# Kernel optimization log

Hardware: AMD Instinct MI355X
Metric: run time of the kernel (lower is better)

## Reference

```python
import jax, jax.numpy as jnp
import numpy as np

N = 100_000   # nodes
E = 1_600_000 # edges (avg degree 16)
D = 32        # feat_dim


def setup_inputs() -> dict:
    key = jax.random.key(0)
    ks = jax.random.split(key, 8)
    scale = 1.0 / np.sqrt(D).astype(np.float32)
    feat = jax.random.normal(ks[0], (N, D), dtype=jnp.float32)
    src = jax.random.randint(ks[1], (E,), 0, N, dtype=jnp.int32)
    dst = jax.random.randint(ks[2], (E,), 0, N, dtype=jnp.int32)
    Ws = jax.random.normal(ks[3], (D, D), dtype=jnp.float32) * scale  # src_trans, no bias
    Wd = jax.random.normal(ks[4], (D, D), dtype=jnp.float32) * scale  # dst_trans
    bd = jax.random.normal(ks[5], (D,), dtype=jnp.float32) * scale
    Wr = jax.random.normal(ks[6], (D, D), dtype=jnp.float32) * scale  # res_trans
    br = jax.random.normal(ks[7], (D,), dtype=jnp.float32) * scale
    return {"feat": feat, "src": src, "dst": dst,
            "Ws": Ws, "Wd": Wd, "bd": bd, "Wr": Wr, "br": br}


def reference(feat, src, dst, Ws, Wd, bd, Wr, br):
    # in-degree of each destination node (constant wrt feat)
    deg = jax.ops.segment_sum(jnp.ones((E,), dtype=feat.dtype), dst,
                              num_segments=N)  # [N]

    # --- message passing: agg[v] = sum_{(u->v)} (src_feat[u] + dst_feat[v]) ---
    src_feat = feat @ Ws.T                      # [N, D]
    dst_feat = feat @ Wd.T + bd                 # [N, D]
    # sum of src contributions via scatter-add; dst contribution = deg[v]*dst_feat[v]
    agg = jax.ops.segment_sum(src_feat[src], dst, num_segments=N) \
          + deg[:, None] * dst_feat             # [N, D]

    out = agg @ Wr.T + br                       # [N, D]  (res_trans)

    # --- apply_edges: out_feat[e] = src2[u_e] + dst2[v_e] ---
    src2 = out @ Ws.T                           # [N, D]
    dst2 = out @ Wd.T + bd                      # [N, D]
    return src2[src] + dst2[dst]                # [E, D]
```

## Files before the change

### kernel.cpp

```cpp
#include <hip/hip_runtime.h>

#define D 32
#define SCHUNK 1024

__global__ __launch_bounds__(256) void k_node_transform(
    const float* __restrict__ feat, const float* __restrict__ Ws,
    const float* __restrict__ Wd, const float* __restrict__ bd,
    float* __restrict__ src_feat, float* __restrict__ dst_feat, int N)
{
    __shared__ float WsT[D * D];
    __shared__ float WdT[D * D];
    __shared__ float bdS[D];
    __shared__ float fS[8][D];

    const int t = threadIdx.x;
    for (int i = t; i < D * D; i += 256) {
        const int d = i >> 5, k = i & 31;
        WsT[k * D + d] = Ws[i];
        WdT[k * D + d] = Wd[i];
    }
    if (t < D) bdS[t] = bd[t];

    const int nodeBase = blockIdx.x * 8;
    {
        const int n = nodeBase + (t >> 5);
        fS[t >> 5][t & 31] = (n < N) ? feat[nodeBase * D + t] : 0.f;
    }
    __syncthreads();

    const int nl = t >> 5, d = t & 31;
    const int n = nodeBase + nl;
    if (n >= N) return;

    float accS = 0.f, accD = bdS[d];
#pragma unroll
    for (int k = 0; k < D; ++k) {
        const float f = fS[nl][k];
        accS += f * WsT[k * D + d];
        accD += f * WdT[k * D + d];
    }
    src_feat[n * D + d] = accS;
    dst_feat[n * D + d] = accD;
}

__global__ __launch_bounds__(256) void k_hist(
    const int* __restrict__ dst, int* __restrict__ deg, int E)
{
    const int e = blockIdx.x * 256 + threadIdx.x;
    if (e < E) atomicAdd(&deg[dst[e]], 1);
}

__global__ __launch_bounds__(256) void k_scan1(
    const int* __restrict__ deg, int* __restrict__ offset,
    int* __restrict__ blockSums, int N)
{
    __shared__ int buf[2][SCHUNK];
    const int t = threadIdx.x;
    const int base = blockIdx.x * SCHUNK;
    for (int j = t; j < SCHUNK; j += 256)
        buf[0][j] = (base + j < N) ? deg[base + j] : 0;
    __syncthreads();
    int pin = 0;
    for (int off = 1; off < SCHUNK; off <<= 1) {
        for (int j = t; j < SCHUNK; j += 256)
            buf[pin ^ 1][j] = buf[pin][j] + (j >= off ? buf[pin][j - off] : 0);
        __syncthreads();
        pin ^= 1;
    }
    for (int j = t; j < SCHUNK; j += 256)
        if (base + j < N) offset[base + j] = (j > 0) ? buf[pin][j - 1] : 0;
    if (t == 0) blockSums[blockIdx.x] = buf[pin][SCHUNK - 1];
}

__global__ __launch_bounds__(64) void k_scan2(int* __restrict__ bs, int nb)
{
    if (threadIdx.x == 0) {
        int run = 0;
        for (int i = 0; i < nb; ++i) { const int v = bs[i]; bs[i] = run; run += v; }
    }
}

__global__ __launch_bounds__(256) void k_scan3(
    int* __restrict__ offset, int* __restrict__ cursor,
    const int* __restrict__ blockSums, int N)
{
    const int i = blockIdx.x * 256 + threadIdx.x;
    if (i < N) {
        const int o = offset[i] + blockSums[i >> 10];
        offset[i] = o;
        cursor[i] = o;
    }
}

__global__ __launch_bounds__(256) void k_scatter_ids(
    const int* __restrict__ src, const int* __restrict__ dst,
    int* __restrict__ cursor, int* __restrict__ edge_src, int E)
{
    const int e = blockIdx.x * 256 + threadIdx.x;
    if (e < E) {
        const int slot = atomicAdd(&cursor[dst[e]], 1);
        edge_src[slot] = src[e];
    }
}

__global__ __launch_bounds__(256) void k_agg_fused(
    const int* __restrict__ edge_src, const int* __restrict__ offset,
    const int* __restrict__ deg,
    const float* __restrict__ src_feat, const float* __restrict__ dst_feat,
    const float* __restrict__ Ws, const float* __restrict__ Wd,
    const float* __restrict__ bd, const float* __restrict__ Wr,
    const float* __restrict__ br,
    float* __restrict__ src2, float* __restrict__ dst2, int N)
{
    __shared__ float WsT[D * D];
    __shared__ float WdT[D * D];
    __shared__ float WrT[D * D];
    __shared__ float bdS[D], brS[D];
    __shared__ float aS[8][D];
    __shared__ float oS[8][D];

    const int t = threadIdx.x;
    for (int i = t; i < D * D; i += 256) {
        const int d = i >> 5, k = i & 31;
        WsT[k * D + d] = Ws[i];
        WdT[k * D + d] = Wd[i];
        WrT[k * D + d] = Wr[i];
    }
    if (t < D) { bdS[t] = bd[t]; brS[t] = br[t]; }

    const int nl = t >> 5, d = t & 31;
    const int n = blockIdx.x * 8 + nl;

    float acc = 0.f;
    if (n < N) {
        const int off = offset[n];
        const int dg  = deg[n];
        for (int i = 0; i < dg; ++i) {
            const int u = edge_src[off + i];
            acc += src_feat[u * D + d];
        }
        acc += (float)dg * dst_feat[n * D + d];
    }
    __syncthreads();

    aS[nl][d] = acc;
    __syncthreads();

    float o = brS[d];
#pragma unroll
    for (int k = 0; k < D; ++k) o += aS[nl][k] * WrT[k * D + d];
    oS[nl][d] = o;
    __syncthreads();

    if (n >= N) return;
    float s = 0.f, dd = bdS[d];
#pragma unroll
    for (int k = 0; k < D; ++k) {
        const float ov = oS[nl][k];
        s  += ov * WsT[k * D + d];
        dd += ov * WdT[k * D + d];
    }
    src2[n * D + d] = s;
    dst2[n * D + d] = dd;
}

__global__ __launch_bounds__(256) void k_gather_out(
    const int* __restrict__ src, const int* __restrict__ dst,
    const float* __restrict__ src2, const float* __restrict__ dst2,
    float* __restrict__ out, int E)
{
    const long g = (long)blockIdx.x * 256 + threadIdx.x;
    const int e = (int)(g >> 3);
    if (e >= E) return;
    const int q = (int)(g & 7);

    const int u = src[e], v = dst[e];
    const float4 a = *(const float4*)(src2 + u * D + q * 4);
    const float4 b = *(const float4*)(dst2 + v * D + q * 4);
    float4 r;
    r.x = a.x + b.x; r.y = a.y + b.y; r.z = a.z + b.z; r.w = a.w + b.w;
    *(float4*)(out + (long)e * D + q * 4) = r;
}

extern "C" void kernel_launch(void* const* d_in, const int* in_sizes, int n_in,
                              void* d_out, int out_size, void* d_ws, size_t ws_size,
                              hipStream_t stream)
{
    const float* feat = (const float*)d_in[0];
    const int*   src  = (const int*)d_in[1];
    const int*   dst  = (const int*)d_in[2];
    const float* Ws   = (const float*)d_in[3];
    const float* Wd   = (const float*)d_in[4];
    const float* bd   = (const float*)d_in[5];
    const float* Wr   = (const float*)d_in[6];
    const float* br   = (const float*)d_in[7];
    float* out = (float*)d_out;

    const int N = in_sizes[0] / D;
    const int E = in_sizes[1];

    const size_t nodeBytes = (size_t)N * D * sizeof(float);

    char* ob = (char*)d_out;
    float* src_feat = (float*)ob;
    float* dst_feat = (float*)(ob + nodeBytes);
    int*   edge_src = (int*)(ob + 2 * nodeBytes);
    int*   deg      = (int*)(ob + 2 * nodeBytes + (size_t)E * 4);
    int*   offset   = deg + N;
    int*   cursor   = offset + N;
    int*   blockSums= cursor + N;

    float* src2 = (float*)d_ws;
    float* dst2 = (float*)((char*)d_ws + nodeBytes);

    const int nodeBlocks = (N + 7) / 8;
    const int edgeThreadBlocks = (E + 255) / 256;
    const int nBlocks256 = (N + 255) / 256;
    const int nbScan = (N + SCHUNK - 1) / SCHUNK;

    hipMemsetAsync(deg, 0, (size_t)N * sizeof(int), stream);

    k_node_transform<<<nodeBlocks, 256, 0, stream>>>(feat, Ws, Wd, bd,
                                                     src_feat, dst_feat, N);

    k_hist<<<edgeThreadBlocks, 256, 0, stream>>>(dst, deg, E);
    k_scan1<<<nbScan, 256, 0, stream>>>(deg, offset, blockSums, N);
    k_scan2<<<1, 64, 0, stream>>>(blockSums, nbScan);
    k_scan3<<<nBlocks256, 256, 0, stream>>>(offset, cursor, blockSums, N);
    k_scatter_ids<<<edgeThreadBlocks, 256, 0, stream>>>(src, dst, cursor,
                                                        edge_src, E);

    k_agg_fused<<<nodeBlocks, 256, 0, stream>>>(edge_src, offset, deg,
                                                src_feat, dst_feat,
                                                Ws, Wd, bd, Wr, br,
                                                src2, dst2, N);

    const long outThreads = (long)E * 8;
    const int outBlocks = (int)((outThreads + 255) / 256);
    k_gather_out<<<outBlocks, 256, 0, stream>>>(src, dst, src2, dst2, out, E);
}
```

Before: 654.5 us.

## Replace per-node CSR with bucketed counting sort and shared-memory aggregation

Swaps the per-node histogram, scan and atomic scatter for a two-level counting sort. Edges are grouped into 128-node buckets using per-block shared-memory histograms, which removes global atomics and shrinks the scan. Aggregation then runs one block per bucket and accumulates neighbour features with shared-memory atomics, packing the local destination id into the high bits of the source id. It also drops the degree memset. The cost is fewer aggregation blocks (about 782), shared-atomic contention, and a packing scheme that assumes fewer than 2^20 nodes.

```diff
diff --git a/kernel.cpp b/kernel.cpp
--- a/kernel.cpp
+++ b/kernel.cpp
@@ -1,6 +1,11 @@
 #include <hip/hip_runtime.h>
 
 #define D 32
+#define BSHIFT 7
+#define BNODES 128
+#define NB_MAX 1024
+#define ACHUNK 16384
+#define ATHREADS 512
 #define SCHUNK 1024
 
 __global__ __launch_bounds__(256) void k_node_transform(
@@ -43,22 +48,32 @@
     dst_feat[n * D + d] = accD;
 }
 
-__global__ __launch_bounds__(256) void k_hist(
-    const int* __restrict__ dst, int* __restrict__ deg, int E)
-{
-    const int e = blockIdx.x * 256 + threadIdx.x;
-    if (e < E) atomicAdd(&deg[dst[e]], 1);
+__global__ __launch_bounds__(ATHREADS) void k_histA(
+    const int* __restrict__ dst, int* __restrict__ cnt,
+    int E, int NB, int nblkA)
+{
+    __shared__ int h[NB_MAX];
+    const int t = threadIdx.x;
+    for (int i = t; i < NB; i += ATHREADS) h[i] = 0;
+    __syncthreads();
+    const int base = blockIdx.x * ACHUNK;
+    const int end = min(base + ACHUNK, E);
+    for (int e = base + t; e < end; e += ATHREADS)
+        atomicAdd(&h[dst[e] >> BSHIFT], 1);
+    __syncthreads();
+    for (int b = t; b < NB; b += ATHREADS)
+        cnt[b * nblkA + blockIdx.x] = h[b];
 }
 
 __global__ __launch_bounds__(256) void k_scan1(
-    const int* __restrict__ deg, int* __restrict__ offset,
-    int* __restrict__ blockSums, int N)
+    const int* __restrict__ in, int* __restrict__ out,
+    int* __restrict__ bsums, int L)
 {
     __shared__ int buf[2][SCHUNK];
     const int t = threadIdx.x;
     const int base = blockIdx.x * SCHUNK;
     for (int j = t; j < SCHUNK; j += 256)
-        buf[0][j] = (base + j < N) ? deg[base + j] : 0;
+        buf[0][j] = (base + j < L) ? in[base + j] : 0;
     __syncthreads();
     int pin = 0;
     for (int off = 1; off < SCHUNK; off <<= 1) {
@@ -68,8 +83,8 @@
         pin ^= 1;
     }
     for (int j = t; j < SCHUNK; j += 256)
-        if (base + j < N) offset[base + j] = (j > 0) ? buf[pin][j - 1] : 0;
-    if (t == 0) blockSums[blockIdx.x] = buf[pin][SCHUNK - 1];
+        if (base + j < L) out[base + j] = (j > 0) ? buf[pin][j - 1] : 0;
+    if (t == 0) bsums[blockIdx.x] = buf[pin][SCHUNK - 1];
 }
 
 __global__ __launch_bounds__(64) void k_scan2(int* __restrict__ bs, int nb)
@@ -81,45 +96,52 @@
 }
 
 __global__ __launch_bounds__(256) void k_scan3(
-    int* __restrict__ offset, int* __restrict__ cursor,
-    const int* __restrict__ blockSums, int N)
+    int* __restrict__ out, const int* __restrict__ bsums, int L)
 {
     const int i = blockIdx.x * 256 + threadIdx.x;
-    if (i < N) {
-        const int o = offset[i] + blockSums[i >> 10];
-        offset[i] = o;
-        cursor[i] = o;
-    }
-}
-
-__global__ __launch_bounds__(256) void k_scatter_ids(
+    if (i < L) out[i] += bsums[i >> 10];
+}
+
+__global__ __launch_bounds__(ATHREADS) void k_scatA(
     const int* __restrict__ src, const int* __restrict__ dst,
-    int* __restrict__ cursor, int* __restrict__ edge_src, int E)
-{
-    const int e = blockIdx.x * 256 + threadIdx.x;
-    if (e < E) {
-        const int slot = atomicAdd(&cursor[dst[e]], 1);
-        edge_src[slot] = src[e];
-    }
-}
-
-__global__ __launch_bounds__(256) void k_agg_fused(
-    const int* __restrict__ edge_src, const int* __restrict__ offset,
-    const int* __restrict__ deg,
+    const int* __restrict__ off, int* __restrict__ edge_pk,
+    int E, int NB, int nblkA)
+{
+    __shared__ int h[NB_MAX];
+    const int t = threadIdx.x;
+    for (int i = t; i < NB; i += ATHREADS) h[i] = 0;
+    __syncthreads();
+    const int base = blockIdx.x * ACHUNK;
+    const int end = min(base + ACHUNK, E);
+    for (int e = base + t; e < end; e += ATHREADS) {
+        const int v = dst[e];
+        const int b = v >> BSHIFT;
+        const int r = atomicAdd(&h[b], 1);
+        const int pos = off[b * nblkA + blockIdx.x] + r;
+        edge_pk[pos] = src[e] | ((v & (BNODES - 1)) << 20);
+    }
+}
+
+__global__ __launch_bounds__(256) void k_aggB(
+    const int* __restrict__ edge_pk, const int* __restrict__ off,
     const float* __restrict__ src_feat, const float* __restrict__ dst_feat,
     const float* __restrict__ Ws, const float* __restrict__ Wd,
     const float* __restrict__ bd, const float* __restrict__ Wr,
     const float* __restrict__ br,
-    float* __restrict__ src2, float* __restrict__ dst2, int N)
-{
+    float* __restrict__ src2, float* __restrict__ dst2,
+    int N, int E, int NB, int nblkA)
+{
+    __shared__ float agg[BNODES][D];
+    __shared__ float oAll[BNODES][D];
     __shared__ float WsT[D * D];
     __shared__ float WdT[D * D];
     __shared__ float WrT[D * D];
     __shared__ float bdS[D], brS[D];
-    __shared__ float aS[8][D];
-    __shared__ float oS[8][D];
-
-    const int t = threadIdx.x;
+    __shared__ int degS[BNODES];
+
+    const int t = threadIdx.x;
+    const int b = blockIdx.x;
+
     for (int i = t; i < D * D; i += 256) {
         const int d = i >> 5, k = i & 31;
         WsT[k * D + d] = Ws[i];
@@ -127,41 +149,56 @@
         WrT[k * D + d] = Wr[i];
     }
     if (t < D) { bdS[t] = bd[t]; brS[t] = br[t]; }
-
-    const int nl = t >> 5, d = t & 31;
-    const int n = blockIdx.x * 8 + nl;
-
-    float acc = 0.f;
-    if (n < N) {
-        const int off = offset[n];
-        const int dg  = deg[n];
-        for (int i = 0; i < dg; ++i) {
-            const int u = edge_src[off + i];
-            acc += src_feat[u * D + d];
+    for (int i = t; i < BNODES * D; i += 256) ((float*)agg)[i] = 0.f;
+    for (int i = t; i < BNODES; i += 256) degS[i] = 0;
+    __syncthreads();
+
+    const int eStart = off[b * nblkA];
+    const int eEnd   = (b == NB - 1) ? E : off[(b + 1) * nblkA];
+
+    const int g = t >> 5, lane = t & 31;
+    for (int i = eStart + g; i < eEnd; i += 8) {
+        const int p = edge_pk[i];
+        const int u = p & 0xFFFFF;
+        const int vloc = p >> 20;
+        atomicAdd(&agg[vloc][lane], src_feat[u * D + lane]);
+        if (lane == 0) atomicAdd(&degS[vloc], 1);
+    }
+    __syncthreads();
+
+    const int nodeBase = b << BSHIFT;
+
+    for (int p = 0; p < BNODES / 8; ++p) {
+        const int nloc = p * 8 + g;
+        const int n = nodeBase + nloc;
+        if (n < N)
+            agg[nloc][lane] += (float)degS[nloc] * dst_feat[n * D + lane];
+    }
+    __syncthreads();
+
+    for (int p = 0; p < BNODES / 8; ++p) {
+        const int nloc = p * 8 + g;
+        float o = brS[lane];
+#pragma unroll
+        for (int k = 0; k < D; ++k) o += agg[nloc][k] * WrT[k * D + lane];
+        oAll[nloc][lane] = o;
+    }
+    __syncthreads();
+
+    for (int p = 0; p < BNODES / 8; ++p) {
+        const int nloc = p * 8 + g;
+        const int n = nodeBase + nloc;
+        if (n >= N) continue;
+        float s = 0.f, dd = bdS[lane];
+#pragma unroll
+        for (int k = 0; k < D; ++k) {
+            const float ov = oAll[nloc][k];
+            s  += ov * WsT[k * D + lane];
+            dd += ov * WdT[k * D + lane];
         }
-        acc += (float)dg * dst_feat[n * D + d];
-    }
-    __syncthreads();
-
-    aS[nl][d] = acc;
-    __syncthreads();
-
-    float o = brS[d];
-#pragma unroll
-    for (int k = 0; k < D; ++k) o += aS[nl][k] * WrT[k * D + d];
-    oS[nl][d] = o;
-    __syncthreads();
-
-    if (n >= N) return;
-    float s = 0.f, dd = bdS[d];
-#pragma unroll
-    for (int k = 0; k < D; ++k) {
-        const float ov = oS[nl][k];
-        s  += ov * WsT[k * D + d];
-        dd += ov * WdT[k * D + d];
-    }
-    src2[n * D + d] = s;
-    dst2[n * D + d] = dd;
+        src2[n * D + lane] = s;
+        dst2[n * D + lane] = dd;
+    }
 }
 
 __global__ __launch_bounds__(256) void k_gather_out(
@@ -199,41 +236,38 @@
     const int N = in_sizes[0] / D;
     const int E = in_sizes[1];
 
+    const int NB    = (N + BNODES - 1) >> BSHIFT;
+    const int nblkA = (E + ACHUNK - 1) / ACHUNK;
+    const int L     = NB * nblkA;
+    const int nbScan = (L + SCHUNK - 1) / SCHUNK;
+
     const size_t nodeBytes = (size_t)N * D * sizeof(float);
 
     char* ob = (char*)d_out;
     float* src_feat = (float*)ob;
     float* dst_feat = (float*)(ob + nodeBytes);
-    int*   edge_src = (int*)(ob + 2 * nodeBytes);
-    int*   deg      = (int*)(ob + 2 * nodeBytes + (size_t)E * 4);
-    int*   offset   = deg + N;
-    int*   cursor   = offset + N;
-    int*   blockSums= cursor + N;
+    int*   edge_pk  = (int*)(ob + 2 * nodeBytes);
+    int*   cnt      = (int*)(ob + 2 * nodeBytes + (size_t)E * 4);
+    int*   off      = cnt + L;
+    int*   bsums    = off + L;
 
     float* src2 = (float*)d_ws;
     float* dst2 = (float*)((char*)d_ws + nodeBytes);
 
     const int nodeBlocks = (N + 7) / 8;
-    const int edgeThreadBlocks = (E + 255) / 256;
-    const int nBlocks256 = (N + 255) / 256;
-    const int nbScan = (N + SCHUNK - 1) / SCHUNK;
-
-    hipMemsetAsync(deg, 0, (size_t)N * sizeof(int), stream);
 
     k_node_transform<<<nodeBlocks, 256, 0, stream>>>(feat, Ws, Wd, bd,
                                                      src_feat, dst_feat, N);
 
-    k_hist<<<edgeThreadBlocks, 256, 0, stream>>>(dst, deg, E);
-    k_scan1<<<nbScan, 256, 0, stream>>>(deg, offset, blockSums, N);
-    k_scan2<<<1, 64, 0, stream>>>(blockSums, nbScan);
-    k_scan3<<<nBlocks256, 256, 0, stream>>>(offset, cursor, blockSums, N);
-    k_scatter_ids<<<edgeThreadBlocks, 256, 0, stream>>>(src, dst, cursor,
-                                                        edge_src, E);
-
-    k_agg_fused<<<nodeBlocks, 256, 0, stream>>>(edge_src, offset, deg,
-                                                src_feat, dst_feat,
-                                                Ws, Wd, bd, Wr, br,
-                                                src2, dst2, N);
+    k_histA<<<nblkA, ATHREADS, 0, stream>>>(dst, cnt, E, NB, nblkA);
+    k_scan1<<<nbScan, 256, 0, stream>>>(cnt, off, bsums, L);
+    k_scan2<<<1, 64, 0, stream>>>(bsums, nbScan);
+    k_scan3<<<(L + 255) / 256, 256, 0, stream>>>(off, bsums, L);
+    k_scatA<<<nblkA, ATHREADS, 0, stream>>>(src, dst, off, edge_pk, E, NB, nblkA);
+
+    k_aggB<<<NB, 256, 0, stream>>>(edge_pk, off, src_feat, dst_feat,
+                                   Ws, Wd, bd, Wr, br, src2, dst2,
+                                   N, E, NB, nblkA);
 
     const long outThreads = (long)E * 8;
     const int outBlocks = (int)((outThreads + 255) / 256);
```

Measured after the change: 824.8 us. 1.26x slower.
